# Performance work log

Measured on AMD Instinct MI355X. Metric: run time of the kernel, lower is better.

The kernel has to match this reference:

```python
import jax, jax.numpy as jnp
import numpy as np

_D, _R = 1024, 4096


def flow_multinomial(n, p):
    """n: [...], p: [..., k] -> mean [..., k], cov [..., k, k]."""
    mean = n[..., None] * p  # [..., k]
    k = p.shape[-1]
    eye = jnp.eye(k, dtype=p.dtype)
    # diag(mean) - n * p p^T
    cov = mean[..., None] * eye - n[..., None, None] * (p[..., :, None] * p[..., None, :])
    return mean, cov


def mvn_logprob(x, mean, cov):
    """Batched MVN log-prob via Cholesky. x/mean: [..., k], cov: [..., k, k]."""
    k = x.shape[-1]
    L = jnp.linalg.cholesky(cov)
    diff = (x - mean)[..., None]  # [..., k, 1]
    z = jax.lax.linalg.triangular_solve(L, diff, left_side=True, lower=True)
    quad = jnp.sum(z[..., 0] ** 2, axis=-1)
    logdet = 2.0 * jnp.sum(jnp.log(jnp.diagonal(L, axis1=-2, axis2=-1)), axis=-1)
    return -0.5 * (k * jnp.log(2.0 * jnp.pi) + logdet + quad)


def setup_inputs() -> dict:
    D, R = _D, _R
    key = jax.random.key(0)
    ks = jax.random.split(key, 20)
    u = lambda k, shape, lo, hi: jax.random.uniform(k, shape, minval=lo, maxval=hi, dtype=jnp.float32)
    N = u(ks[0], (R,), 1e6, 2e6)
    S = N * u(ks[1], (D, R), 0.4, 0.7)
    E = N * u(ks[2], (D, R), 0.005, 0.02)
    I = N * u(ks[3], (D, R), 0.005, 0.02)
    T = N * u(ks[4], (D, R), 0.002, 0.01)
    # observed flows for each transition (any finite values are valid)
    S_E = S[:-1] * u(ks[5], (D - 1, R), 0.0, 0.02)
    E_I = E[:-1] * u(ks[6], (D - 1, R), 0.1, 0.4)
    I_T = I[:-1] * u(ks[7], (D - 1, R), 0.1, 0.3)
    I_U = I[:-1] * u(ks[8], (D - 1, R), 0.1, 0.3)
    T_R = T[:-1] * u(ks[9], (D - 1, R), 0.2, 0.5)
    T_D = T[:-1] * u(ks[10], (D - 1, R), 0.0, 0.05)
    adjacency = u(ks[11], (R, R), 0.0, 1.0)
    logit_decay_E = jax.random.normal(ks[12], (), dtype=jnp.float32)
    logit_decay_I = jax.random.normal(ks[13], (), dtype=jnp.float32)
    logit_decay_T = jax.random.normal(ks[14], (), dtype=jnp.float32)
    detection_rate = u(ks[15], (D, R), 0.05, 0.95)
    recovery_rate = u(ks[16], (D, R), 0.05, 0.95)
    contagion_I = u(ks[17], (D, R), 0.1, 2.0)
    return dict(S=S, E=E, I=I, T=T, N=N, S_E=S_E, E_I=E_I, I_T=I_T, I_U=I_U,
                T_R=T_R, T_D=T_D, adjacency=adjacency,
                logit_decay_E=logit_decay_E, logit_decay_I=logit_decay_I,
                logit_decay_T=logit_decay_T, detection_rate=detection_rate,
                recovery_rate=recovery_rate, contagion_I=contagion_I)


def reference(S, E, I, T, N, S_E, E_I, I_T, I_U, T_R, T_D, adjacency,
              logit_decay_E, logit_decay_I, logit_decay_T,
              detection_rate, recovery_rate, contagion_I):
    decay_E = jax.nn.sigmoid(logit_decay_E)
    decay_I = jax.nn.sigmoid(logit_decay_I)
    decay_T = jax.nn.sigmoid(logit_decay_T)

    # states at the start of each transition t = 0 .. D-2
    So, Eo, Io, To = S[:-1], E[:-1], I[:-1], T[:-1]  # [D-1, R]

    # prob_S_E, vectorized over transitions: A @ I_t for each t
    AI = jnp.einsum('rq,tq->tr', adjacency, Io)       # [D-1, R]
    AN = adjacency @ N                                 # [R]
    p_SE = -jnp.expm1(-(contagion_I[:-1] * AI) / AN)   # [D-1, R]

    # S -> E (1-dim MVN)
    mS, cS = flow_multinomial(So, p_SE[..., None])
    lpS = mvn_logprob(S_E[..., None], mS, cS)

    # E -> I (1-dim MVN)
    p_EI = jnp.broadcast_to(decay_E, p_SE.shape)
    mE, cE = flow_multinomial(Eo, p_EI[..., None])
    lpE = mvn_logprob(E_I[..., None], mE, cE)

    # I -> (T, U) (2-dim MVN)
    det = detection_rate[:-1]
    pI = jnp.stack([det * decay_I, (1.0 - det) * decay_I], axis=-1)  # [D-1, R, 2]
    mI, cI = flow_multinomial(Io, pI)
    lpI = mvn_logprob(jnp.stack([I_T, I_U], axis=-1), mI, cI)

    # T -> (R, D) (2-dim MVN)
    rec = recovery_rate[:-1]
    pT = jnp.stack([rec * decay_T, (1.0 - rec) * decay_T], axis=-1)
    mT, cT = flow_multinomial(To, pT)
    lpT = mvn_logprob(jnp.stack([T_R, T_D], axis=-1), mT, cT)

    # sum over transitions -> per-region total log prob [R]
    return jnp.sum(lpS + lpE + lpI + lpT, axis=0)
```

## Files before the change

### kernel.cpp

```cpp
#include <hip/hip_runtime.h>
#include <hip/hip_bf16.h>
#include <math.h>

typedef __attribute__((ext_vector_type(8))) short bf16x8;
typedef __attribute__((ext_vector_type(4))) float f32x4;

__device__ inline ushort f2bf(float x) {
  union { float f; unsigned u; } c; c.f = x;
  unsigned u = c.u;
  u += 0x7fffu + ((u >> 16) & 1u);
  return (ushort)(u >> 16);
}

__global__ __launch_bounds__(256) void conv_I_kernel(const float* __restrict__ in,
                                                     ushort* __restrict__ out, int n) {
  int i = (blockIdx.x * 256 + threadIdx.x) * 4;
  if (i + 3 < n) {
    float4 v = *(const float4*)(in + i);
    ushort4 o;
    o.x = f2bf(v.x); o.y = f2bf(v.y); o.z = f2bf(v.z); o.w = f2bf(v.w);
    *(ushort4*)(out + i) = o;
  }
}

__global__ __launch_bounds__(256) void conv_adj_an(const float* __restrict__ adj,
                                                   const float* __restrict__ Nv,
                                                   ushort* __restrict__ adjbf,
                                                   float* __restrict__ AN, int R) {
  const int r = blockIdx.x;
  const int tid = threadIdx.x;
  const float* row = adj + (size_t)r * R;
  ushort* orow = adjbf + (size_t)r * R;
  float acc = 0.f;
  for (int q0 = tid * 4; q0 < R; q0 += 256 * 4) {
    float4 v = *(const float4*)(row + q0);
    float4 nv = *(const float4*)(Nv + q0);
    acc += v.x * nv.x + v.y * nv.y + v.z * nv.z + v.w * nv.w;
    ushort4 o;
    o.x = f2bf(v.x); o.y = f2bf(v.y); o.z = f2bf(v.z); o.w = f2bf(v.w);
    *(ushort4*)(orow + q0) = o;
  }
  #pragma unroll
  for (int off = 32; off > 0; off >>= 1) acc += __shfl_down(acc, off, 64);
  __shared__ float red[4];
  if ((tid & 63) == 0) red[tid >> 6] = acc;
  __syncthreads();
  if (tid == 0) AN[r] = red[0] + red[1] + red[2] + red[3];
}

__global__ __launch_bounds__(256) void gemm_bt_kernel(const ushort* __restrict__ A,
                                                      const ushort* __restrict__ B,
                                                      float* __restrict__ C,
                                                      int M, int N, int K) {
  __shared__ __align__(16) ushort sA[128 * 32];
  __shared__ __align__(16) ushort sB[128 * 32];
  const int tid = threadIdx.x;
  const int bn = blockIdx.x, bm = blockIdx.y;
  const int wave = tid >> 6, lane = tid & 63;
  const int wm = (wave >> 1) * 64, wn = (wave & 1) * 64;
  const int srow = tid >> 1, scol = (tid & 1) * 16;
  const size_t Arow = (size_t)(bm * 128 + srow) * K + scol;
  const size_t Brow = (size_t)(bn * 128 + srow) * K + scol;
  const int fm = lane & 15, fk = (lane >> 4) * 8;

  f32x4 acc[4][4];
  #pragma unroll
  for (int i = 0; i < 4; ++i)
    #pragma unroll
    for (int j = 0; j < 4; ++j) acc[i][j] = (f32x4){0.f, 0.f, 0.f, 0.f};

  for (int k0 = 0; k0 < K; k0 += 32) {
    __syncthreads();
    uint4 a0 = *(const uint4*)(A + Arow + k0);
    uint4 a1 = *(const uint4*)(A + Arow + k0 + 8);
    uint4 b0 = *(const uint4*)(B + Brow + k0);
    uint4 b1 = *(const uint4*)(B + Brow + k0 + 8);
    *(uint4*)(sA + srow * 32 + scol) = a0;
    *(uint4*)(sA + srow * 32 + scol + 8) = a1;
    *(uint4*)(sB + srow * 32 + scol) = b0;
    *(uint4*)(sB + srow * 32 + scol + 8) = b1;
    __syncthreads();
    bf16x8 af[4], bfr[4];
    #pragma unroll
    for (int i = 0; i < 4; ++i)
      af[i] = *(const bf16x8*)(sA + (wm + i * 16 + fm) * 32 + fk);
    #pragma unroll
    for (int j = 0; j < 4; ++j)
      bfr[j] = *(const bf16x8*)(sB + (wn + j * 16 + fm) * 32 + fk);
    #pragma unroll
    for (int i = 0; i < 4; ++i)
      #pragma unroll
      for (int j = 0; j < 4; ++j)
        acc[i][j] = __builtin_amdgcn_mfma_f32_16x16x32_bf16(af[i], bfr[j], acc[i][j], 0, 0, 0);
  }

  const int cm = (lane >> 4) * 4, cn = lane & 15;
  #pragma unroll
  for (int i = 0; i < 4; ++i)
    #pragma unroll
    for (int j = 0; j < 4; ++j) {
      size_t base = (size_t)(bm * 128 + wm + i * 16 + cm) * N + (bn * 128 + wn + j * 16 + cn);
      #pragma unroll
      for (int v = 0; v < 4; ++v)
        C[base + (size_t)v * N] = acc[i][j][v];
    }
}

__global__ __launch_bounds__(256) void logprob_kernel(
    const float* __restrict__ S, const float* __restrict__ E,
    const float* __restrict__ I, const float* __restrict__ T,
    const float* __restrict__ S_E, const float* __restrict__ E_I,
    const float* __restrict__ I_T, const float* __restrict__ I_U,
    const float* __restrict__ T_R, const float* __restrict__ T_D,
    const float* __restrict__ detr, const float* __restrict__ recr,
    const float* __restrict__ cont, const float* __restrict__ AI,
    const float* __restrict__ AN,
    const float* __restrict__ pldE, const float* __restrict__ pldI,
    const float* __restrict__ pldT, float* __restrict__ out, int D1, int R) {
  const int r = blockIdx.x * 256 + threadIdx.x;
  if (r >= R) return;
  const float dE = 1.f / (1.f + expf(-pldE[0]));
  const float dI = 1.f / (1.f + expf(-pldI[0]));
  const float dT = 1.f / (1.f + expf(-pldT[0]));
  const float an = AN[r];
  const float L2PI = 1.8378770664093453f;
  const float omE = 1.f - dE;
  const float omI = 1.f - dI;
  const float omT = 1.f - dT;
  float acc = 0.f;
  const int t0 = blockIdx.y * 16;
  const int t1 = min(t0 + 16, D1);
  for (int t = t0; t < t1; ++t) {
    const size_t idx = (size_t)t * R + r;
    {
      float n_ = S[idx];
      float p = -expm1f(-(cont[idx] * AI[idx]) / an);
      float m = n_ * p;
      float var = m * (1.f - p);
      float d = S_E[idx] - m;
      acc += __logf(var) + d * d / var;
    }
    {
      float n_ = E[idx];
      float m = n_ * dE;
      float var = m * omE;
      float d = E_I[idx] - m;
      acc += __logf(var) + d * d / var;
    }
    {
      float n_ = I[idx];
      float de = detr[idx];
      float p1 = de * dI, p2 = (1.f - de) * dI;
      float d1 = I_T[idx] - n_ * p1;
      float d2 = I_U[idx] - n_ * p2;
      float den = n_ * p1 * p2 * omI;
      float quad = (d1 * d1 * p2 * (1.f - p2) + 2.f * d1 * d2 * p1 * p2 +
                    d2 * d2 * p1 * (1.f - p1)) / den;
      acc += __logf(n_ * den) + quad;
    }
    {
      float n_ = T[idx];
      float re = recr[idx];
      float p1 = re * dT, p2 = (1.f - re) * dT;
      float d1 = T_R[idx] - n_ * p1;
      float d2 = T_D[idx] - n_ * p2;
      float den = n_ * p1 * p2 * omT;
      float quad = (d1 * d1 * p2 * (1.f - p2) + 2.f * d1 * d2 * p1 * p2 +
                    d2 * d2 * p1 * (1.f - p1)) / den;
      acc += __logf(n_ * den) + quad;
    }
  }
  float partial = -0.5f * acc - 3.f * L2PI * (float)(t1 - t0);
  atomicAdd(&out[r], partial);
}

extern "C" void kernel_launch(void* const* d_in, const int* in_sizes, int n_in,
                              void* d_out, int out_size, void* d_ws, size_t ws_size,
                              hipStream_t stream) {
  const float* S    = (const float*)d_in[0];
  const float* E    = (const float*)d_in[1];
  const float* I    = (const float*)d_in[2];
  const float* T    = (const float*)d_in[3];
  const float* Nv   = (const float*)d_in[4];
  const float* S_E  = (const float*)d_in[5];
  const float* E_I  = (const float*)d_in[6];
  const float* I_T  = (const float*)d_in[7];
  const float* I_U  = (const float*)d_in[8];
  const float* T_R  = (const float*)d_in[9];
  const float* T_D  = (const float*)d_in[10];
  const float* adj  = (const float*)d_in[11];
  const float* ldE  = (const float*)d_in[12];
  const float* ldI  = (const float*)d_in[13];
  const float* ldT  = (const float*)d_in[14];
  const float* detr = (const float*)d_in[15];
  const float* recr = (const float*)d_in[16];
  const float* cont = (const float*)d_in[17];
  float* out = (float*)d_out;

  const int R  = in_sizes[4];
  const int D  = in_sizes[0] / R;
  const int D1 = D - 1;

  char* ws = (char*)d_ws;
  ushort* adjbf = (ushort*)ws;
  ushort* Ibf   = (ushort*)(ws + (size_t)R * R * 2);
  float*  AIbuf = (float*)(ws + (size_t)R * R * 2 + (size_t)D * R * 2);
  float*  ANbuf = (float*)((char*)AIbuf + (size_t)D * R * 4);

  const int nI = D * R;
  hipLaunchKernelGGL(conv_I_kernel, dim3(nI / 4 / 256), dim3(256), 0, stream, I, Ibf, nI);
  hipLaunchKernelGGL(conv_adj_an, dim3(R), dim3(256), 0, stream, adj, Nv, adjbf, ANbuf, R);
  hipLaunchKernelGGL(gemm_bt_kernel, dim3(R / 128, D / 128), dim3(256), 0, stream,
                     Ibf, adjbf, AIbuf, D, R, R);
  hipMemsetAsync(d_out, 0, (size_t)out_size * sizeof(float), stream);
  hipLaunchKernelGGL(logprob_kernel, dim3(R / 256, (D1 + 15) / 16), dim3(256), 0, stream,
                     S, E, I, T, S_E, E_I, I_T, I_U, T_R, T_D, detr, recr, cont,
                     AIbuf, ANbuf, ldE, ldI, ldT, out, D1, R);
}
```

Baseline: 400.2 us.

## Split-K GEMM with direct global-to-LDS loads and vectorized logprob kernel

The GEMM is split into two K halves along grid z, each writing its own partial AI buffer. Tiles are staged with global_load_lds direct-to-LDS loads instead of register round-trips. The logprob kernel now handles four regions per thread with float4 loads and sums the two partial AI buffers. This doubles the GEMM grid to fill more CUs and cuts load-instruction overhead, at the cost of writing and reading an extra D×R fp32 buffer.

```diff
diff --git a/kernel.cpp b/kernel.cpp
--- a/kernel.cpp
+++ b/kernel.cpp
@@ -4,12 +4,19 @@
 
 typedef __attribute__((ext_vector_type(8))) short bf16x8;
 typedef __attribute__((ext_vector_type(4))) float f32x4;
+typedef unsigned int u32;
 
 __device__ inline ushort f2bf(float x) {
   union { float f; unsigned u; } c; c.f = x;
   unsigned u = c.u;
   u += 0x7fffu + ((u >> 16) & 1u);
   return (ushort)(u >> 16);
+}
+
+__device__ __forceinline__ void gl_lds16(const ushort* g, ushort* l) {
+  __builtin_amdgcn_global_load_lds(
+      (const __attribute__((address_space(1))) u32*)g,
+      (__attribute__((address_space(3))) u32*)l, 16, 0, 0);
 }
 
 __global__ __launch_bounds__(256) void conv_I_kernel(const float* __restrict__ in,
@@ -48,19 +55,30 @@
   if (tid == 0) AN[r] = red[0] + red[1] + red[2] + red[3];
 }
 
-__global__ __launch_bounds__(256) void gemm_bt_kernel(const ushort* __restrict__ A,
-                                                      const ushort* __restrict__ B,
-                                                      float* __restrict__ C,
-                                                      int M, int N, int K) {
+__global__ __launch_bounds__(256) void gemm_bt_lds(const ushort* __restrict__ A,
+                                                   const ushort* __restrict__ B,
+                                                   float* __restrict__ C,
+                                                   int M, int N, int K, int Khalf) {
   __shared__ __align__(16) ushort sA[128 * 32];
   __shared__ __align__(16) ushort sB[128 * 32];
   const int tid = threadIdx.x;
-  const int bn = blockIdx.x, bm = blockIdx.y;
+  const int bn = blockIdx.x, bm = blockIdx.y, bz = blockIdx.z;
   const int wave = tid >> 6, lane = tid & 63;
   const int wm = (wave >> 1) * 64, wn = (wave & 1) * 64;
-  const int srow = tid >> 1, scol = (tid & 1) * 16;
-  const size_t Arow = (size_t)(bm * 128 + srow) * K + scol;
-  const size_t Brow = (size_t)(bn * 128 + srow) * K + scol;
+
+  const int p0 = wave * 2, p1 = wave * 2 + 1;
+  const int lrow = lane >> 2;
+  const int scol = (lane & 3) * 8;
+  const size_t kbase = (size_t)bz * Khalf + scol;
+  const ushort* Ag0 = A + (size_t)(bm * 128 + p0 * 16 + lrow) * K + kbase;
+  const ushort* Ag1 = A + (size_t)(bm * 128 + p1 * 16 + lrow) * K + kbase;
+  const ushort* Bg0 = B + (size_t)(bn * 128 + p0 * 16 + lrow) * K + kbase;
+  const ushort* Bg1 = B + (size_t)(bn * 128 + p1 * 16 + lrow) * K + kbase;
+  ushort* sA0 = sA + p0 * 16 * 32;
+  ushort* sA1 = sA + p1 * 16 * 32;
+  ushort* sB0 = sB + p0 * 16 * 32;
+  ushort* sB1 = sB + p1 * 16 * 32;
+
   const int fm = lane & 15, fk = (lane >> 4) * 8;
 
   f32x4 acc[4][4];
@@ -69,16 +87,12 @@
     #pragma unroll
     for (int j = 0; j < 4; ++j) acc[i][j] = (f32x4){0.f, 0.f, 0.f, 0.f};
 
-  for (int k0 = 0; k0 < K; k0 += 32) {
+  for (int k0 = 0; k0 < Khalf; k0 += 32) {
     __syncthreads();
-    uint4 a0 = *(const uint4*)(A + Arow + k0);
-    uint4 a1 = *(const uint4*)(A + Arow + k0 + 8);
-    uint4 b0 = *(const uint4*)(B + Brow + k0);
-    uint4 b1 = *(const uint4*)(B + Brow + k0 + 8);
-    *(uint4*)(sA + srow * 32 + scol) = a0;
-    *(uint4*)(sA + srow * 32 + scol + 8) = a1;
-    *(uint4*)(sB + srow * 32 + scol) = b0;
-    *(uint4*)(sB + srow * 32 + scol + 8) = b1;
+    gl_lds16(Ag0 + k0, sA0);
+    gl_lds16(Ag1 + k0, sA1);
+    gl_lds16(Bg0 + k0, sB0);
+    gl_lds16(Bg1 + k0, sB1);
     __syncthreads();
     bf16x8 af[4], bfr[4];
     #pragma unroll
@@ -94,6 +108,7 @@
         acc[i][j] = __builtin_amdgcn_mfma_f32_16x16x32_bf16(af[i], bfr[j], acc[i][j], 0, 0, 0);
   }
 
+  float* Cz = C + (size_t)bz * M * N;
   const int cm = (lane >> 4) * 4, cn = lane & 15;
   #pragma unroll
   for (int i = 0; i < 4; ++i)
@@ -102,8 +117,49 @@
       size_t base = (size_t)(bm * 128 + wm + i * 16 + cm) * N + (bn * 128 + wn + j * 16 + cn);
       #pragma unroll
       for (int v = 0; v < 4; ++v)
-        C[base + (size_t)v * N] = acc[i][j][v];
+        Cz[base + (size_t)v * N] = acc[i][j][v];
     }
+}
+
+__device__ __forceinline__ float elem_ll(float Sv, float Ev, float Iv, float Tv,
+                                         float sev, float eiv, float itv, float iuv,
+                                         float trv, float tdv, float dev, float rev,
+                                         float cov, float aiv, float an_,
+                                         float dE, float omE, float dI, float omI,
+                                         float dT, float omT) {
+  float acc;
+  {
+    float p = -expm1f(-(cov * aiv) / an_);
+    float m = Sv * p;
+    float var = m * (1.f - p);
+    float d = sev - m;
+    acc = __logf(var) + d * d / var;
+  }
+  {
+    float m = Ev * dE;
+    float var = m * omE;
+    float d = eiv - m;
+    acc += __logf(var) + d * d / var;
+  }
+  {
+    float p1 = dev * dI, p2 = (1.f - dev) * dI;
+    float d1 = itv - Iv * p1;
+    float d2 = iuv - Iv * p2;
+    float den = Iv * p1 * p2 * omI;
+    float quad = (d1 * d1 * p2 * (1.f - p2) + 2.f * d1 * d2 * p1 * p2 +
+                  d2 * d2 * p1 * (1.f - p1)) / den;
+    acc += __logf(Iv * den) + quad;
+  }
+  {
+    float p1 = rev * dT, p2 = (1.f - rev) * dT;
+    float d1 = trv - Tv * p1;
+    float d2 = tdv - Tv * p2;
+    float den = Tv * p1 * p2 * omT;
+    float quad = (d1 * d1 * p2 * (1.f - p2) + 2.f * d1 * d2 * p1 * p2 +
+                  d2 * d2 * p1 * (1.f - p1)) / den;
+    acc += __logf(Tv * den) + quad;
+  }
+  return acc;
 }
 
 __global__ __launch_bounds__(256) void logprob_kernel(
@@ -113,65 +169,57 @@
     const float* __restrict__ I_T, const float* __restrict__ I_U,
     const float* __restrict__ T_R, const float* __restrict__ T_D,
     const float* __restrict__ detr, const float* __restrict__ recr,
-    const float* __restrict__ cont, const float* __restrict__ AI,
-    const float* __restrict__ AN,
+    const float* __restrict__ cont, const float* __restrict__ AI0,
+    const float* __restrict__ AI1, const float* __restrict__ AN,
     const float* __restrict__ pldE, const float* __restrict__ pldI,
     const float* __restrict__ pldT, float* __restrict__ out, int D1, int R) {
-  const int r = blockIdx.x * 256 + threadIdx.x;
-  if (r >= R) return;
+  const int r0 = (blockIdx.x * 256 + threadIdx.x) * 4;
+  if (r0 + 3 >= R + 3 - 3 && r0 >= R) return;
   const float dE = 1.f / (1.f + expf(-pldE[0]));
   const float dI = 1.f / (1.f + expf(-pldI[0]));
   const float dT = 1.f / (1.f + expf(-pldT[0]));
-  const float an = AN[r];
+  const float omE = 1.f - dE, omI = 1.f - dI, omT = 1.f - dT;
   const float L2PI = 1.8378770664093453f;
-  const float omE = 1.f - dE;
-  const float omI = 1.f - dI;
-  const float omT = 1.f - dT;
-  float acc = 0.f;
+  float4 an4 = *(const float4*)(AN + r0);
+  float an_[4] = {an4.x, an4.y, an4.z, an4.w};
+  float acc[4] = {0.f, 0.f, 0.f, 0.f};
   const int t0 = blockIdx.y * 16;
   const int t1 = min(t0 + 16, D1);
   for (int t = t0; t < t1; ++t) {
-    const size_t idx = (size_t)t * R + r;
-    {
-      float n_ = S[idx];
-      float p = -expm1f(-(cont[idx] * AI[idx]) / an);
-      float m = n_ * p;
-      float var = m * (1.f - p);
-      float d = S_E[idx] - m;
-      acc += __logf(var) + d * d / var;
-    }
-    {
-      float n_ = E[idx];
-      float m = n_ * dE;
-      float var = m * omE;
-      float d = E_I[idx] - m;
-      acc += __logf(var) + d * d / var;
-    }
-    {
-      float n_ = I[idx];
-      float de = detr[idx];
-      float p1 = de * dI, p2 = (1.f - de) * dI;
-      float d1 = I_T[idx] - n_ * p1;
-      float d2 = I_U[idx] - n_ * p2;
-      float den = n_ * p1 * p2 * omI;
-      float quad = (d1 * d1 * p2 * (1.f - p2) + 2.f * d1 * d2 * p1 * p2 +
-                    d2 * d2 * p1 * (1.f - p1)) / den;
-      acc += __logf(n_ * den) + quad;
-    }
-    {
-      float n_ = T[idx];
-      float re = recr[idx];
-      float p1 = re * dT, p2 = (1.f - re) * dT;
-      float d1 = T_R[idx] - n_ * p1;
-      float d2 = T_D[idx] - n_ * p2;
-      float den = n_ * p1 * p2 * omT;
-      float quad = (d1 * d1 * p2 * (1.f - p2) + 2.f * d1 * d2 * p1 * p2 +
-                    d2 * d2 * p1 * (1.f - p1)) / den;
-      acc += __logf(n_ * den) + quad;
-    }
-  }
-  float partial = -0.5f * acc - 3.f * L2PI * (float)(t1 - t0);
-  atomicAdd(&out[r], partial);
+    const size_t idx = (size_t)t * R + r0;
+    float4 Sv = *(const float4*)(S + idx);
+    float4 Ev = *(const float4*)(E + idx);
+    float4 Iv = *(const float4*)(I + idx);
+    float4 Tv = *(const float4*)(T + idx);
+    float4 se = *(const float4*)(S_E + idx);
+    float4 ei = *(const float4*)(E_I + idx);
+    float4 it = *(const float4*)(I_T + idx);
+    float4 iu = *(const float4*)(I_U + idx);
+    float4 tr = *(const float4*)(T_R + idx);
+    float4 td = *(const float4*)(T_D + idx);
+    float4 de = *(const float4*)(detr + idx);
+    float4 re = *(const float4*)(recr + idx);
+    float4 co = *(const float4*)(cont + idx);
+    float4 a0 = *(const float4*)(AI0 + idx);
+    float4 a1 = *(const float4*)(AI1 + idx);
+    float ai[4] = {a0.x + a1.x, a0.y + a1.y, a0.z + a1.z, a0.w + a1.w};
+    float Sa[4] = {Sv.x, Sv.y, Sv.z, Sv.w}, Ea[4] = {Ev.x, Ev.y, Ev.z, Ev.w};
+    float Ia[4] = {Iv.x, Iv.y, Iv.z, Iv.w}, Ta[4] = {Tv.x, Tv.y, Tv.z, Tv.w};
+    float sea[4] = {se.x, se.y, se.z, se.w}, eia[4] = {ei.x, ei.y, ei.z, ei.w};
+    float ita[4] = {it.x, it.y, it.z, it.w}, iua[4] = {iu.x, iu.y, iu.z, iu.w};
+    float tra[4] = {tr.x, tr.y, tr.z, tr.w}, tda[4] = {td.x, td.y, td.z, td.w};
+    float dea[4] = {de.x, de.y, de.z, de.w}, rea[4] = {re.x, re.y, re.z, re.w};
+    float coa[4] = {co.x, co.y, co.z, co.w};
+    #pragma unroll
+    for (int v = 0; v < 4; ++v)
+      acc[v] += elem_ll(Sa[v], Ea[v], Ia[v], Ta[v], sea[v], eia[v], ita[v], iua[v],
+                        tra[v], tda[v], dea[v], rea[v], coa[v], ai[v], an_[v],
+                        dE, omE, dI, omI, dT, omT);
+  }
+  const float cterm = -3.f * L2PI * (float)(t1 - t0);
+  #pragma unroll
+  for (int v = 0; v < 4; ++v)
+    atomicAdd(&out[r0 + v], -0.5f * acc[v] + cterm);
 }
 
 extern "C" void kernel_launch(void* const* d_in, const int* in_sizes, int n_in,
@@ -205,15 +253,15 @@
   ushort* adjbf = (ushort*)ws;
   ushort* Ibf   = (ushort*)(ws + (size_t)R * R * 2);
   float*  AIbuf = (float*)(ws + (size_t)R * R * 2 + (size_t)D * R * 2);
-  float*  ANbuf = (float*)((char*)AIbuf + (size_t)D * R * 4);
+  float*  ANbuf = (float*)((char*)AIbuf + 2 * (size_t)D * R * 4);
 
   const int nI = D * R;
   hipLaunchKernelGGL(conv_I_kernel, dim3(nI / 4 / 256), dim3(256), 0, stream, I, Ibf, nI);
   hipLaunchKernelGGL(conv_adj_an, dim3(R), dim3(256), 0, stream, adj, Nv, adjbf, ANbuf, R);
-  hipLaunchKernelGGL(gemm_bt_kernel, dim3(R / 128, D / 128), dim3(256), 0, stream,
-                     Ibf, adjbf, AIbuf, D, R, R);
+  hipLaunchKernelGGL(gemm_bt_lds, dim3(R / 128, D / 128, 2), dim3(256), 0, stream,
+                     Ibf, adjbf, AIbuf, D, R, R, R / 2);
   hipMemsetAsync(d_out, 0, (size_t)out_size * sizeof(float), stream);
-  hipLaunchKernelGGL(logprob_kernel, dim3(R / 256, (D1 + 15) / 16), dim3(256), 0, stream,
+  hipLaunchKernelGGL(logprob_kernel, dim3(R / 1024, (D1 + 15) / 16), dim3(256), 0, stream,
                      S, E, I, T, S_E, E_I, I_T, I_U, T_R, T_D, detr, recr, cont,
-                     AIbuf, ANbuf, ldE, ldI, ldT, out, D1, R);
-}
+                     AIbuf, AIbuf + (size_t)D * R, ANbuf, ldE, ldI, ldT, out, D1, R);
+}
```

After: 385.1 us. 1.04x faster.
